# Kernel tuning notes

Hardware: AMD Instinct MI355X
Metric: run time of the kernel (lower is better)

## Reference

```python
import jax, jax.numpy as jnp
import numpy as np

EMBED_DIM = 768
FFN_DIM = 3072
N_WIRES = 10


def setup_inputs() -> dict:
    key = jax.random.key(0)
    ks = jax.random.split(key, 7)
    x = jax.random.normal(ks[0], (8, 2048, EMBED_DIM), dtype=jnp.float32)
    # map_to_wires: nn.Linear(embed_dim, n_wires, bias=False) -> weight [n_wires, embed_dim]
    W_map = jax.random.normal(ks[1], (N_WIRES, EMBED_DIM), dtype=jnp.float32) / np.sqrt(EMBED_DIM)
    # trainable RY rotation angles, one per wire
    theta = jax.random.uniform(ks[2], (N_WIRES,), dtype=jnp.float32, minval=-np.pi, maxval=np.pi)
    W1 = jax.random.normal(ks[3], (FFN_DIM, N_WIRES), dtype=jnp.float32) / np.sqrt(N_WIRES)
    b1 = jnp.zeros((FFN_DIM,), dtype=jnp.float32)
    W2 = jax.random.normal(ks[4], (EMBED_DIM, FFN_DIM), dtype=jnp.float32) / np.sqrt(FFN_DIM)
    b2 = jnp.zeros((EMBED_DIM,), dtype=jnp.float32)
    return {"x": x, "W_map": W_map, "theta": theta, "W1": W1, "b1": b1, "W2": W2, "b2": b2}


def reference(x, W_map, theta, W1, b1, W2, b2):
    batch, seq_len, embed_dim = x.shape
    x_flat = x.reshape(batch * seq_len, embed_dim)            # [F, E]
    x_wires = x_flat @ W_map.T                                 # [F, W]
    # Quantum circuit: per wire i, state RY(theta_i) RX(x_i) |0>.
    # All gates are single-qubit on the |0...0> product state, so the
    # register stays a product state and <Z_i> reduces exactly to
    # cos(theta_i) * cos(x_i) (same math as the full 2^n statevector sim).
    q_out = jnp.cos(theta)[None, :] * jnp.cos(x_wires)         # [F, W]
    h = jax.nn.relu(q_out @ W1.T + b1)                         # [F, FFN]
    out = h @ W2.T + b2                                        # [F, E]
    return out.reshape(batch, seq_len, embed_dim)
```

## Files before the change

### kernel.cpp

```cpp
#include <hip/hip_runtime.h>
#include <hip/hip_bf16.h>


typedef __attribute__((ext_vector_type(4))) float f32x4;
typedef __attribute__((ext_vector_type(8))) short bf16x8;

#define F_TOTAL 16384
#define E_DIM   768
#define FFN     3072

static __device__ __forceinline__ unsigned short f2bf(float f) {
    union { float f; unsigned int i; } v; v.f = f;
    unsigned int r = v.i + 0x7FFFu + ((v.i >> 16) & 1u);
    return (unsigned short)(r >> 16);
}
static __device__ __forceinline__ unsigned int pkbf(float a, float b) {
    __hip_bfloat162 h2 = __float22bfloat162_rn(float2{a, b});
    union { __hip_bfloat162 h; unsigned int u; } v; v.h = h2; return v.u;
}
static __device__ __forceinline__ void gload16(const void* g, void* l) {
    __builtin_amdgcn_global_load_lds((const __attribute__((address_space(1))) unsigned int*)g,
                                     (__attribute__((address_space(3))) unsigned int*)l,
                                     16, 0, 0);
}

__global__ __launch_bounds__(384) void kW2(const float* __restrict__ w2,
                                           unsigned short* __restrict__ w2b) {
    const int n = (int)blockIdx.x;
    const int c = (int)threadIdx.x;
    const float4* src = (const float4*)(w2 + (size_t)n * FFN + c * 8);
    float4 a = src[0], b = src[1];
    bf16x8 v;
    v[0] = (short)f2bf(a.x); v[1] = (short)f2bf(a.y);
    v[2] = (short)f2bf(a.z); v[3] = (short)f2bf(a.w);
    v[4] = (short)f2bf(b.x); v[5] = (short)f2bf(b.y);
    v[6] = (short)f2bf(b.z); v[7] = (short)f2bf(b.w);
    *(bf16x8*)(w2b + (size_t)n * FFN + (size_t)(c ^ (n & 7)) * 8) = v;
}

__global__ void kP(const float* __restrict__ w1,
                   const float* __restrict__ b1,
                   unsigned short* __restrict__ w1p) {
    int k = blockIdx.x * 256 + threadIdx.x;
    if (k >= FFN) return;
    float r[32];
#pragma unroll
    for (int w = 0; w < 10; ++w) r[w] = w1[k * 10 + w];
    r[10] = b1[k];
#pragma unroll
    for (int w = 11; w < 32; ++w) r[w] = 0.f;
#pragma unroll
    for (int c = 0; c < 4; ++c) {
        bf16x8 v;
#pragma unroll
        for (int e = 0; e < 8; ++e) v[e] = (short)f2bf(r[c * 8 + e]);
        *(bf16x8*)(w1p + (size_t)k * 32 + (size_t)((c ^ (k & 3)) * 8)) = v;
    }
}

__global__ __launch_bounds__(256) void kQ(const float* __restrict__ x,
                                          const float* __restrict__ wm,
                                          const float* __restrict__ th,
                                          unsigned short* __restrict__ qp) {
    __shared__ float wms[10 * 768];
    const int tid = (int)threadIdx.x;
    for (int i = tid; i < 10 * 768; i += 256) wms[i] = wm[i];
    __syncthreads();

    const int wv = tid >> 6, l = tid & 63;
    const int mbase = (int)blockIdx.x * 16 + wv * 4;
    const float thv = (l < 10) ? th[l] : 0.f;
    const float cth = __cosf(thv);

#pragma unroll
    for (int r = 0; r < 4; ++r) {
        const int m = mbase + r;
        const float4* xp = (const float4*)(x + (size_t)m * E_DIM);
        const float4 xa = xp[l], xb = xp[64 + l], xc = xp[128 + l];
        float s[10];
#pragma unroll
        for (int w = 0; w < 10; ++w) {
            const float4* wp = (const float4*)(wms + w * E_DIM);
            const float4 wa = wp[l], wb = wp[64 + l], wc = wp[128 + l];
            float t0 = xa.x * wa.x;
            float t1 = xa.y * wa.y;
            t0 = fmaf(xa.z, wa.z, t0); t1 = fmaf(xa.w, wa.w, t1);
            t0 = fmaf(xb.x, wb.x, t0); t1 = fmaf(xb.y, wb.y, t1);
            t0 = fmaf(xb.z, wb.z, t0); t1 = fmaf(xb.w, wb.w, t1);
            t0 = fmaf(xc.x, wc.x, t0); t1 = fmaf(xc.y, wc.y, t1);
            t0 = fmaf(xc.z, wc.z, t0); t1 = fmaf(xc.w, wc.w, t1);
            s[w] = t0 + t1;
        }
#pragma unroll
        for (int w = 0; w < 10; ++w) {
            float v = s[w];
            v += __shfl_xor(v, 1);  v += __shfl_xor(v, 2);  v += __shfl_xor(v, 4);
            v += __shfl_xor(v, 8);  v += __shfl_xor(v, 16); v += __shfl_xor(v, 32);
            s[w] = v;
        }
        if (l < 32) {
            float sv = 0.f;
#pragma unroll
            for (int w = 0; w < 10; ++w) sv = (l == w) ? s[w] : sv;
            float val = (l < 10) ? (cth * __cosf(sv)) : ((l == 10) ? 1.0f : 0.f);
            qp[(size_t)m * 32 + (size_t)((((l >> 3) ^ (m & 3)) * 8) + (l & 7))] = f2bf(val);
        }
    }
}

__global__ __launch_bounds__(512, 4) void kG(const unsigned short* __restrict__ w2b,
                                             const float* __restrict__ b2,
                                             const unsigned short* __restrict__ qp,
                                             const unsigned short* __restrict__ w1p,
                                             float* __restrict__ outp) {
    __shared__ __align__(16) unsigned short w2s[2][192 * 64];
    __shared__ __align__(16) unsigned short hs[128 * 64];

    const int tid = (int)threadIdx.x;
    const int wv = tid >> 6, l = tid & 63;
    const int bid = (int)blockIdx.x;
    const int x8 = bid & 7, yb = bid >> 3;
    const int m0 = ((x8 & 1) * 64 + yb) * 128;
    const int n0 = (x8 >> 1) * 192;

    const int rw = tid >> 3, cw = tid & 7;
    const int wr = wv >> 2, wc = wv & 3;

    int hwo[4];
    {
        const int hm = wv * 16 + (l & 15);
        const int kb = (l >> 4) * 4;
#pragma unroll
        for (int ki = 0; ki < 4; ++ki) {
            int k = ki * 16 + kb;
            int c = k >> 3;
            hwo[ki] = hm * 64 + ((c ^ (hm & 7)) * 8) + (k & 7);
        }
    }

#define STAGE(BUF, KT) do { int k0_ = (KT) * 64;                                   \
    _Pragma("unroll") for (int i_ = 0; i_ < 3; ++i_) {                             \
        int r_ = i_ * 64 + rw;                                                     \
        gload16(w2b + (size_t)(n0 + r_) * FFN + k0_ + (size_t)cw * 8,              \
                (unsigned short*)w2s[BUF] + i_ * 4096 + wv * 512); } } while (0)

#define LOADW1(D, KT, KI) do {                                                     \
    const unsigned short* a_ = w1p + (size_t)((KT) * 64 + (KI) * 16 + (l & 15)) * 32 \
                                   + (size_t)(((l >> 4) ^ (l & 3)) * 8);           \
    asm volatile("global_load_dwordx4 %0, %1, off" : "=v"(D) : "v"(a_)); } while (0)

    bf16x8 aq;
    {
        const unsigned short* qa = qp + (size_t)(m0 + wv * 16 + (l & 15)) * 32
                                      + (size_t)(((l >> 4) ^ (l & 3)) * 8);
        asm volatile("global_load_dwordx4 %0, %1, off" : "=v"(aq) : "v"(qa));
    }
    bf16x8 f0, f1, f2, f3, g0, g1, g2, g3;
    STAGE(0, 0);
    LOADW1(f0, 0, 0); LOADW1(f1, 0, 1); LOADW1(f2, 0, 2); LOADW1(f3, 0, 3);

    const f32x4 z4 = {0.f, 0.f, 0.f, 0.f};
    f32x4 acc[4][3];
#pragma unroll
    for (int a = 0; a < 4; ++a)
#pragma unroll
        for (int b = 0; b < 3; ++b) acc[a][b] = z4;

    int cur = 0;
    for (int t = 0; t < 48; ++t) {
        asm volatile("s_waitcnt vmcnt(0)" ::: "memory");
        __builtin_amdgcn_sched_barrier(0);
        __builtin_amdgcn_s_barrier();
        __builtin_amdgcn_sched_barrier(0);

        if (t < 47) {
            STAGE(cur ^ 1, t + 1);
            LOADW1(g0, t + 1, 0); LOADW1(g1, t + 1, 1);
            LOADW1(g2, t + 1, 2); LOADW1(g3, t + 1, 3);
        }

        {
            f32x4 hv0 = __builtin_amdgcn_mfma_f32_16x16x32_bf16(f0, aq, z4, 0, 0, 0);
            f32x4 hv1 = __builtin_amdgcn_mfma_f32_16x16x32_bf16(f1, aq, z4, 0, 0, 0);
            f32x4 hv2 = __builtin_amdgcn_mfma_f32_16x16x32_bf16(f2, aq, z4, 0, 0, 0);
            f32x4 hv3 = __builtin_amdgcn_mfma_f32_16x16x32_bf16(f3, aq, z4, 0, 0, 0);
            uint2 pw;
            pw.x = pkbf(fmaxf(hv0[0], 0.f), fmaxf(hv0[1], 0.f));
            pw.y = pkbf(fmaxf(hv0[2], 0.f), fmaxf(hv0[3], 0.f));
            *(uint2*)(hs + hwo[0]) = pw;
            pw.x = pkbf(fmaxf(hv1[0], 0.f), fmaxf(hv1[1], 0.f));
            pw.y = pkbf(fmaxf(hv1[2], 0.f), fmaxf(hv1[3], 0.f));
            *(uint2*)(hs + hwo[1]) = pw;
            pw.x = pkbf(fmaxf(hv2[0], 0.f), fmaxf(hv2[1], 0.f));
            pw.y = pkbf(fmaxf(hv2[2], 0.f), fmaxf(hv2[3], 0.f));
            *(uint2*)(hs + hwo[2]) = pw;
            pw.x = pkbf(fmaxf(hv3[0], 0.f), fmaxf(hv3[1], 0.f));
            pw.y = pkbf(fmaxf(hv3[2], 0.f), fmaxf(hv3[3], 0.f));
            *(uint2*)(hs + hwo[3]) = pw;
        }

        asm volatile("s_waitcnt lgkmcnt(0)" ::: "memory");
        __builtin_amdgcn_sched_barrier(0);
        __builtin_amdgcn_s_barrier();
        __builtin_amdgcn_sched_barrier(0);

        {
            const unsigned short* w2c = (const unsigned short*)w2s[cur];
#pragma unroll
            for (int kk2 = 0; kk2 < 2; ++kk2) {
                const int kc = kk2 * 4 + (l >> 4);
                bf16x8 af[4], bfr[3];
#pragma unroll
                for (int mi = 0; mi < 4; ++mi) {
                    int m_ = wr * 64 + mi * 16 + (l & 15);
                    af[mi] = *(const bf16x8*)(hs + m_ * 64 + ((kc ^ (m_ & 7)) * 8));
                }
#pragma unroll
                for (int ni = 0; ni < 3; ++ni) {
                    int n_ = wc * 48 + ni * 16 + (l & 15);
                    bfr[ni] = *(const bf16x8*)(w2c + n_ * 64 + ((kc ^ (n_ & 7)) * 8));
                }
                __builtin_amdgcn_s_setprio(1);
#pragma unroll
                for (int ni = 0; ni < 3; ++ni)
#pragma unroll
                    for (int mi = 0; mi < 4; ++mi)
                        acc[mi][ni] = __builtin_amdgcn_mfma_f32_16x16x32_bf16(af[mi], bfr[ni], acc[mi][ni], 0, 0, 0);
                __builtin_amdgcn_s_setprio(0);
            }
        }

        f0 = g0; f1 = g1; f2 = g2; f3 = g3;
        cur ^= 1;
    }
#undef STAGE
#undef LOADW1

#pragma unroll
    for (int ni = 0; ni < 3; ++ni) {
        int n = n0 + wc * 48 + ni * 16 + (l & 15);
        float b2v = b2[n];
#pragma unroll
        for (int mi = 0; mi < 4; ++mi) {
            int mb = m0 + wr * 64 + mi * 16 + (l >> 4) * 4;
#pragma unroll
            for (int jj = 0; jj < 4; ++jj)
                outp[(size_t)(mb + jj) * E_DIM + n] = acc[mi][ni][jj] + b2v;
        }
    }
}

extern "C" void kernel_launch(void* const* d_in, const int* in_sizes, int n_in,
                              void* d_out, int out_size, void* d_ws, size_t ws_size,
                              hipStream_t stream) {
    const float* x    = (const float*)d_in[0];
    const float* wmap = (const float*)d_in[1];
    const float* th   = (const float*)d_in[2];
    const float* w1   = (const float*)d_in[3];
    const float* b1   = (const float*)d_in[4];
    const float* w2   = (const float*)d_in[5];
    const float* b2   = (const float*)d_in[6];
    float* out = (float*)d_out;

    unsigned short* qp  = (unsigned short*)d_ws;
    unsigned short* w1p = qp + (size_t)F_TOTAL * 32;
    unsigned short* w2b = w1p + (size_t)FFN * 32;

    kW2<<<E_DIM, 384, 0, stream>>>(w2, w2b);
    kP<<<(FFN + 255) / 256, 256, 0, stream>>>(w1, b1, w1p);
    kQ<<<1024, 256, 0, stream>>>(x, wmap, th, qp);
    kG<<<512, 512, 0, stream>>>(w2b, b2, qp, w1p, out);
}
```

Baseline: 124.2 us.

## Merge three preprocessing kernels into one launch and stagger LDS k-window order

```diff
diff --git a/kernel.cpp b/kernel.cpp
--- a/kernel.cpp
+++ b/kernel.cpp
@@ -24,51 +24,62 @@
                                      16, 0, 0);
 }
 
-__global__ __launch_bounds__(384) void kW2(const float* __restrict__ w2,
-                                           unsigned short* __restrict__ w2b) {
-    const int n = (int)blockIdx.x;
-    const int c = (int)threadIdx.x;
-    const float4* src = (const float4*)(w2 + (size_t)n * FFN + c * 8);
-    float4 a = src[0], b = src[1];
-    bf16x8 v;
-    v[0] = (short)f2bf(a.x); v[1] = (short)f2bf(a.y);
-    v[2] = (short)f2bf(a.z); v[3] = (short)f2bf(a.w);
-    v[4] = (short)f2bf(b.x); v[5] = (short)f2bf(b.y);
-    v[6] = (short)f2bf(b.z); v[7] = (short)f2bf(b.w);
-    *(bf16x8*)(w2b + (size_t)n * FFN + (size_t)(c ^ (n & 7)) * 8) = v;
-}
-
-__global__ void kP(const float* __restrict__ w1,
-                   const float* __restrict__ b1,
-                   unsigned short* __restrict__ w1p) {
-    int k = blockIdx.x * 256 + threadIdx.x;
-    if (k >= FFN) return;
-    float r[32];
-#pragma unroll
-    for (int w = 0; w < 10; ++w) r[w] = w1[k * 10 + w];
-    r[10] = b1[k];
-#pragma unroll
-    for (int w = 11; w < 32; ++w) r[w] = 0.f;
-#pragma unroll
-    for (int c = 0; c < 4; ++c) {
-        bf16x8 v;
-#pragma unroll
-        for (int e = 0; e < 8; ++e) v[e] = (short)f2bf(r[c * 8 + e]);
-        *(bf16x8*)(w1p + (size_t)k * 32 + (size_t)((c ^ (k & 3)) * 8)) = v;
-    }
-}
-
-__global__ __launch_bounds__(256) void kQ(const float* __restrict__ x,
-                                          const float* __restrict__ wm,
-                                          const float* __restrict__ th,
-                                          unsigned short* __restrict__ qp) {
+__global__ __launch_bounds__(256) void kPre(const float* __restrict__ x,
+                                            const float* __restrict__ wm,
+                                            const float* __restrict__ th,
+                                            const float* __restrict__ w1,
+                                            const float* __restrict__ b1,
+                                            const float* __restrict__ w2,
+                                            unsigned short* __restrict__ w2b,
+                                            unsigned short* __restrict__ w1p,
+                                            unsigned short* __restrict__ qp) {
     __shared__ float wms[10 * 768];
+    const int bid = (int)blockIdx.x;
     const int tid = (int)threadIdx.x;
+
+    if (bid < 768) {
+        const int n = bid;
+#pragma unroll
+        for (int c0 = 0; c0 < 2; ++c0) {
+            int c = tid + c0 * 256;
+            if (c < 384) {
+                const float4* src = (const float4*)(w2 + (size_t)n * FFN + c * 8);
+                float4 a = src[0], b = src[1];
+                bf16x8 v;
+                v[0] = (short)f2bf(a.x); v[1] = (short)f2bf(a.y);
+                v[2] = (short)f2bf(a.z); v[3] = (short)f2bf(a.w);
+                v[4] = (short)f2bf(b.x); v[5] = (short)f2bf(b.y);
+                v[6] = (short)f2bf(b.z); v[7] = (short)f2bf(b.w);
+                *(bf16x8*)(w2b + (size_t)n * FFN + (size_t)(c ^ (n & 7)) * 8) = v;
+            }
+        }
+        return;
+    }
+    if (bid < 780) {
+        int k = (bid - 768) * 256 + tid;
+        if (k < FFN) {
+            float r[32];
+#pragma unroll
+            for (int w = 0; w < 10; ++w) r[w] = w1[k * 10 + w];
+            r[10] = b1[k];
+#pragma unroll
+            for (int w = 11; w < 32; ++w) r[w] = 0.f;
+#pragma unroll
+            for (int c = 0; c < 4; ++c) {
+                bf16x8 v;
+#pragma unroll
+                for (int e = 0; e < 8; ++e) v[e] = (short)f2bf(r[c * 8 + e]);
+                *(bf16x8*)(w1p + (size_t)k * 32 + (size_t)((c ^ (k & 3)) * 8)) = v;
+            }
+        }
+        return;
+    }
+
     for (int i = tid; i < 10 * 768; i += 256) wms[i] = wm[i];
     __syncthreads();
 
     const int wv = tid >> 6, l = tid & 63;
-    const int mbase = (int)blockIdx.x * 16 + wv * 4;
+    const int mbase = (bid - 780) * 16 + wv * 4;
     const float thv = (l < 10) ? th[l] : 0.f;
     const float cth = __cosf(thv);
 
@@ -125,6 +136,7 @@
 
     const int rw = tid >> 3, cw = tid & 7;
     const int wr = wv >> 2, wc = wv & 3;
+    const int par = wv & 1;
 
     int hwo[4];
     {
@@ -207,8 +219,9 @@
         {
             const unsigned short* w2c = (const unsigned short*)w2s[cur];
 #pragma unroll
-            for (int kk2 = 0; kk2 < 2; ++kk2) {
-                const int kc = kk2 * 4 + (l >> 4);
+            for (int kx = 0; kx < 2; ++kx) {
+                const int win = kx ^ par;
+                const int kc = win * 4 + (l >> 4);
                 bf16x8 af[4], bfr[3];
 #pragma unroll
                 for (int mi = 0; mi < 4; ++mi) {
@@ -266,8 +279,6 @@
     unsigned short* w1p = qp + (size_t)F_TOTAL * 32;
     unsigned short* w2b = w1p + (size_t)FFN * 32;
 
-    kW2<<<E_DIM, 384, 0, stream>>>(w2, w2b);
-    kP<<<(FFN + 255) / 256, 256, 0, stream>>>(w1, b1, w1p);
-    kQ<<<1024, 256, 0, stream>>>(x, wmap, th, qp);
+    kPre<<<1804, 256, 0, stream>>>(x, wmap, th, w1, b1, w2, w2b, w1p, qp);
     kG<<<512, 512, 0, stream>>>(w2b, b2, qp, w1p, out);
 }
```

Result: faster. 120.2 us (-3.2%).
